# Optimization experiments

Measured on AMD Instinct MI355X. Metric: run time of the kernel, lower is better.

Reference implementation:

```python
import jax, jax.numpy as jnp
import numpy as np

N_EMBD = 1024
N_HEAD = 16


def setup_inputs() -> dict:
    key = jax.random.key(0)
    k1, k2, k3 = jax.random.split(key, 3)
    B, T, C = 4, 2048, N_EMBD
    x = jax.random.normal(k1, (B, T, C), dtype=jnp.float32)
    # params (bias=False)
    w_attn = jax.random.normal(k2, (C, 3 * C), dtype=jnp.float32) * (C ** -0.5)
    w_proj = jax.random.normal(k3, (C, C), dtype=jnp.float32) * (C ** -0.5)
    return {"x": x, "w_attn": w_attn, "w_proj": w_proj}


def reference(x, w_attn, w_proj):
    B, T, C = x.shape
    H = N_HEAD
    hs = C // H
    qkv = x @ w_attn  # [B,T,3C]
    q, k, v = jnp.split(qkv, 3, axis=-1)
    # [B,H,T,hs]
    q = q.reshape(B, T, H, hs).transpose(0, 2, 1, 3)
    k = k.reshape(B, T, H, hs).transpose(0, 2, 1, 3)
    v = v.reshape(B, T, H, hs).transpose(0, 2, 1, 3)
    wei = jnp.einsum('bhqd,bhkd->bhqk', q, k) * (hs ** -0.5)
    causal = jnp.tril(jnp.ones((T, T), dtype=bool))
    wei = jnp.where(causal[None, None], wei, -jnp.inf)
    wei = jax.nn.softmax(wei, axis=-1)
    # dropout p=0.0 -> identity
    y = jnp.einsum('bhqk,bhkd->bhqd', wei, v)
    y = y.transpose(0, 2, 1, 3).reshape(B, T, C)
    return y @ w_proj
```

## Files before the change

### kernel.cpp

```cpp
#include <hip/hip_runtime.h>
#include <math.h>
#include <stdint.h>

#define B_BATCH 4
#define T_SEQ   2048
#define C_EMB   1024
#define NH      16
#define HS      64

typedef _Float16 half_t;
typedef __attribute__((ext_vector_type(8))) _Float16 half8;
typedef __attribute__((ext_vector_type(4))) _Float16 half4;
typedef __attribute__((ext_vector_type(2))) __fp16 pk16x2;
typedef __attribute__((ext_vector_type(4))) float f32x4;

static __device__ __forceinline__ f32x4 mfma_k16(half4 a, half4 b, f32x4 c) {
#if __has_builtin(__builtin_amdgcn_mfma_f32_16x16x16f16)
    return __builtin_amdgcn_mfma_f32_16x16x16f16(a, b, c, 0, 0, 0);
#else
    half8 a8 = {a.x, a.y, a.z, a.w, (_Float16)0, (_Float16)0, (_Float16)0, (_Float16)0};
    half8 b8 = {b.x, b.y, b.z, b.w, (_Float16)0, (_Float16)0, (_Float16)0, (_Float16)0};
    return __builtin_amdgcn_mfma_f32_16x16x32_f16(a8, b8, c, 0, 0, 0);
#endif
}

static __device__ __forceinline__ void stage16(const void* g, void* lds_base) {
#if __has_builtin(__builtin_amdgcn_global_load_lds)
    __builtin_amdgcn_global_load_lds(
        (const __attribute__((address_space(1))) void*)g,
        (__attribute__((address_space(3))) void*)lds_base, 16, 0, 0);
#else
    const int lane = threadIdx.x & 63;
    ((uint4*)lds_base)[lane] = *(const uint4*)g;
#endif
}

__global__ __launch_bounds__(256) void prep_kernel(const float* __restrict__ x,
                                                   half_t* __restrict__ xh,
                                                   const float* __restrict__ wa,
                                                   half_t* __restrict__ waT,
                                                   const float* __restrict__ wp,
                                                   half_t* __restrict__ wpT) {
    const int blk = blockIdx.x;
    const int tid = threadIdx.x;

    if (blk < 4096) {
        const int i = blk * 256 + tid;
        const float4 a = *(const float4*)(x + (size_t)i * 8);
        const float4 b = *(const float4*)(x + (size_t)i * 8 + 4);
        const pk16x2 h0 = __builtin_amdgcn_cvt_pkrtz(a.x, a.y);
        const pk16x2 h1 = __builtin_amdgcn_cvt_pkrtz(a.z, a.w);
        const pk16x2 h2 = __builtin_amdgcn_cvt_pkrtz(b.x, b.y);
        const pk16x2 h3 = __builtin_amdgcn_cvt_pkrtz(b.z, b.w);
        half8 o = {(_Float16)h0.x, (_Float16)h0.y, (_Float16)h1.x, (_Float16)h1.y,
                   (_Float16)h2.x, (_Float16)h2.y, (_Float16)h3.x, (_Float16)h3.y};
        *(half8*)(xh + (size_t)i * 8) = o;
        return;
    }

    const float* W;
    half_t* WT;
    int K, N, bb;
    if (blk < 4096 + 768) {
        bb = blk - 4096; W = wa; WT = waT; K = 1024; N = 3072;
    } else {
        bb = blk - 4864; W = wp; WT = wpT; K = 1024; N = 1024;
    }
    const int ntiles = N / 64;
    const int n0 = (bb % ntiles) * 64;
    const int k0 = (bb / ntiles) * 64;

    __shared__ float t[64][65];
    const int r = tid >> 4, c4 = (tid & 15) * 4;
#pragma unroll
    for (int p = 0; p < 4; ++p) {
        const float4 g = *(const float4*)(W + (size_t)(k0 + p * 16 + r) * N + n0 + c4);
        t[p * 16 + r][c4 + 0] = g.x;
        t[p * 16 + r][c4 + 1] = g.y;
        t[p * 16 + r][c4 + 2] = g.z;
        t[p * 16 + r][c4 + 3] = g.w;
    }
    __syncthreads();
#pragma unroll
    for (int p = 0; p < 4; ++p) {
        const int n = p * 16 + r;
        half4 s = {(_Float16)t[c4 + 0][n], (_Float16)t[c4 + 1][n],
                   (_Float16)t[c4 + 2][n], (_Float16)t[c4 + 3][n]};
        *(half4*)(WT + (size_t)(n0 + n) * K + k0 + c4) = s;
    }
}

#define BK2 64

__global__ __launch_bounds__(512, 2) void gemm256(const half_t* __restrict__ A,
                                                  const half_t* __restrict__ Bt,
                                                  half_t* __restrict__ Cout,
                                                  int M, int N, int K) {
    __shared__ __align__(16) half_t SM[65536];

    const int tid  = threadIdx.x;
    const int lane = tid & 63;
    const int wid  = tid >> 6;
    const int l16  = lane & 15;
    const int quad = lane >> 4;

    const int nwg = gridDim.x;
    const int cpx = nwg >> 3;
    const int bid = (blockIdx.x & 7) * cpx + (blockIdx.x >> 3);
    const int nbx = N >> 8;
    const int bx = bid % nbx;
    const int by = bid / nbx;
    const size_t m0 = (size_t)by << 8;
    const size_t n0 = (size_t)bx << 8;

    const int warpM = (wid >> 2) * 128;
    const int wn    = (wid & 3) * 64;
    const int NTk   = K >> 6;

    const int srow = tid >> 3;
    const int scsw = (tid & 7) ^ (srow & 7);
    const half_t* gAs = A  + (m0 + srow) * (size_t)K + scsw * 8;
    const half_t* gBs = Bt + (n0 + srow) * (size_t)K + scsw * 8;

    f32x4 acc[8][4];
#pragma unroll
    for (int i = 0; i < 8; ++i)
#pragma unroll
        for (int j = 0; j < 4; ++j) acc[i][j] = (f32x4){0.f, 0.f, 0.f, 0.f};

    auto ldA = [&](const half_t* Ab, int mt, int kk) -> half8 {
        const int r = warpM + mt * 16 + l16;
        const int c = (kk * 4 + quad) ^ (l16 & 7);
        return *(const half8*)(Ab + r * 64 + c * 8);
    };
    auto ldB = [&](const half_t* Bb, int nt, int kk) -> half8 {
        const int r = wn + nt * 16 + l16;
        const int c = (kk * 4 + quad) ^ (l16 & 7);
        return *(const half8*)(Bb + r * 64 + c * 8);
    };

#pragma unroll
    for (int s = 0; s < 4; ++s)
        stage16(gAs + (size_t)(s * 64) * K, SM + s * 4096 + wid * 512);
#pragma unroll
    for (int s = 0; s < 4; ++s)
        stage16(gBs + (size_t)(s * 64) * K, SM + 16384 + s * 4096 + wid * 512);
    if (NTk > 1) {
#pragma unroll
        for (int s = 0; s < 4; ++s)
            stage16(gBs + (size_t)(s * 64) * K + BK2, SM + 49152 + s * 4096 + wid * 512);
        asm volatile("s_waitcnt vmcnt(4)" ::: "memory");
    } else {
        asm volatile("s_waitcnt vmcnt(0)" ::: "memory");
    }
    __builtin_amdgcn_s_barrier();
    __builtin_amdgcn_sched_barrier(0);

    auto tile_body = [&](int t, half_t* Ac, half_t* Bc, half_t* An) {
        const int kA = (t + 1) * BK2;
        const int kB = (t + 2) * BK2;
        const bool doA = (t + 1) < NTk;
        const bool doB = (t + 2) < NTk;

        half8 fb[4][2];

        if (doA) {
            stage16(gAs + (size_t)(0 * 64) * K + kA, An + 0 * 4096 + wid * 512);
            stage16(gAs + (size_t)(1 * 64) * K + kA, An + 1 * 4096 + wid * 512);
        }
#pragma unroll
        for (int nt = 0; nt < 4; ++nt) {
            fb[nt][0] = ldB(Bc, nt, 0);
            fb[nt][1] = ldB(Bc, nt, 1);
        }
        {
            half8 a00 = ldA(Ac, 0, 0), a01 = ldA(Ac, 0, 1);
            half8 a10 = ldA(Ac, 1, 0), a11 = ldA(Ac, 1, 1);
            __builtin_amdgcn_s_barrier();
            __builtin_amdgcn_s_setprio(1);
#pragma unroll
            for (int nt = 0; nt < 4; ++nt) {
                acc[0][nt] = __builtin_amdgcn_mfma_f32_16x16x32_f16(a00, fb[nt][0], acc[0][nt], 0, 0, 0);
                acc[0][nt] = __builtin_amdgcn_mfma_f32_16x16x32_f16(a01, fb[nt][1], acc[0][nt], 0, 0, 0);
                acc[1][nt] = __builtin_amdgcn_mfma_f32_16x16x32_f16(a10, fb[nt][0], acc[1][nt], 0, 0, 0);
                acc[1][nt] = __builtin_amdgcn_mfma_f32_16x16x32_f16(a11, fb[nt][1], acc[1][nt], 0, 0, 0);
            }
            __builtin_amdgcn_s_setprio(0);
        }
        if (doA) {
            stage16(gAs + (size_t)(2 * 64) * K + kA, An + 2 * 4096 + wid * 512);
            stage16(gAs + (size_t)(3 * 64) * K + kA, An + 3 * 4096 + wid * 512);
        }
        {
            half8 a00 = ldA(Ac, 2, 0), a01 = ldA(Ac, 2, 1);
            half8 a10 = ldA(Ac, 3, 0), a11 = ldA(Ac, 3, 1);
            __builtin_amdgcn_s_barrier();
            __builtin_amdgcn_s_setprio(1);
#pragma unroll
            for (int nt = 0; nt < 4; ++nt) {
                acc[2][nt] = __builtin_amdgcn_mfma_f32_16x16x32_f16(a00, fb[nt][0], acc[2][nt], 0, 0, 0);
                acc[2][nt] = __builtin_amdgcn_mfma_f32_16x16x32_f16(a01, fb[nt][1], acc[2][nt], 0, 0, 0);
                acc[3][nt] = __builtin_amdgcn_mfma_f32_16x16x32_f16(a10, fb[nt][0], acc[3][nt], 0, 0, 0);
                acc[3][nt] = __builtin_amdgcn_mfma_f32_16x16x32_f16(a11, fb[nt][1], acc[3][nt], 0, 0, 0);
            }
            __builtin_amdgcn_s_setprio(0);
        }
        if (doB) {
            stage16(gBs + (size_t)(0 * 64) * K + kB, Bc + 0 * 4096 + wid * 512);
            stage16(gBs + (size_t)(1 * 64) * K + kB, Bc + 1 * 4096 + wid * 512);
        }
        {
            half8 a00 = ldA(Ac, 4, 0), a01 = ldA(Ac, 4, 1);
            half8 a10 = ldA(Ac, 5, 0), a11 = ldA(Ac, 5, 1);
            __builtin_amdgcn_s_barrier();
            __builtin_amdgcn_s_setprio(1);
#pragma unroll
            for (int nt = 0; nt < 4; ++nt) {
                acc[4][nt] = __builtin_amdgcn_mfma_f32_16x16x32_f16(a00, fb[nt][0], acc[4][nt], 0, 0, 0);
                acc[4][nt] = __builtin_amdgcn_mfma_f32_16x16x32_f16(a01, fb[nt][1], acc[4][nt], 0, 0, 0);
                acc[5][nt] = __builtin_amdgcn_mfma_f32_16x16x32_f16(a10, fb[nt][0], acc[5][nt], 0, 0, 0);
                acc[5][nt] = __builtin_amdgcn_mfma_f32_16x16x32_f16(a11, fb[nt][1], acc[5][nt], 0, 0, 0);
            }
            __builtin_amdgcn_s_setprio(0);
        }
        if (doB) {
            stage16(gBs + (size_t)(2 * 64) * K + kB, Bc + 2 * 4096 + wid * 512);
            stage16(gBs + (size_t)(3 * 64) * K + kB, Bc + 3 * 4096 + wid * 512);
        }
        {
            half8 a00 = ldA(Ac, 6, 0), a01 = ldA(Ac, 6, 1);
            half8 a10 = ldA(Ac, 7, 0), a11 = ldA(Ac, 7, 1);
            __builtin_amdgcn_s_barrier();
            __builtin_amdgcn_s_setprio(1);
#pragma unroll
            for (int nt = 0; nt < 4; ++nt) {
                acc[6][nt] = __builtin_amdgcn_mfma_f32_16x16x32_f16(a00, fb[nt][0], acc[6][nt], 0, 0, 0);
                acc[6][nt] = __builtin_amdgcn_mfma_f32_16x16x32_f16(a01, fb[nt][1], acc[6][nt], 0, 0, 0);
                acc[7][nt] = __builtin_amdgcn_mfma_f32_16x16x32_f16(a10, fb[nt][0], acc[7][nt], 0, 0, 0);
                acc[7][nt] = __builtin_amdgcn_mfma_f32_16x16x32_f16(a11, fb[nt][1], acc[7][nt], 0, 0, 0);
            }
            __builtin_amdgcn_s_setprio(0);
        }
        if (doB) {
            asm volatile("s_waitcnt vmcnt(4)" ::: "memory");
        } else if (doA) {
            asm volatile("s_waitcnt vmcnt(0)" ::: "memory");
        }
        __builtin_amdgcn_s_barrier();
        __builtin_amdgcn_sched_barrier(0);
    };

    for (int tt = 0; tt < NTk; tt += 2) {
        tile_body(tt, SM, SM + 16384, SM + 32768);
        if (tt + 1 < NTk)
            tile_body(tt + 1, SM + 32768, SM + 49152, SM);
    }

    __syncthreads();
    float* cw = (float*)SM + wid * 1024;
    const int rrow = lane >> 2;
    const int cseg = (lane & 3) * 16;
#pragma unroll
    for (int mt = 0; mt < 8; ++mt) {
#pragma unroll
        for (int nt = 0; nt < 4; ++nt)
            *(f32x4*)&cw[(nt * 16 + l16) * 16 + quad * 4] = acc[mt][nt];
        half_t tmp[16];
#pragma unroll
        for (int jj = 0; jj < 16; ++jj)
            tmp[jj] = (half_t)cw[(cseg + jj) * 16 + rrow];
        half_t* dst = Cout + (m0 + warpM + mt * 16 + rrow) * (size_t)N + n0 + wn + cseg;
        *(half8*)(dst)     = *(const half8*)(tmp);
        *(half8*)(dst + 8) = *(const half8*)(tmp + 8);
    }
}

__global__ __launch_bounds__(256) void gemm_bt_a64(const half_t* __restrict__ A,
                                                   const half_t* __restrict__ Bt,
                                                   float* __restrict__ Cout,
                                                   int M, int N, int K) {
    __shared__ half_t As[64 * 32];
    __shared__ half_t Bs[128 * 32];

    const int tid  = threadIdx.x;
    const int lane = tid & 63;
    const int wid  = tid >> 6;
    const int l16  = lane & 15;
    const int quad = lane >> 4;

    const int m0 = blockIdx.y * 64;
    const int n0 = blockIdx.x * 128;
    const int wm = (wid & 1) * 32;
    const int wn = (wid >> 1) * 64;

    const half_t* gA  = A  + (size_t)(m0 + wid * 16      + (lane >> 2)) * K + (lane & 3) * 8;
    const half_t* gB0 = Bt + (size_t)(n0 + wid * 16      + (lane >> 2)) * K + (lane & 3) * 8;
    const half_t* gB1 = Bt + (size_t)(n0 + wid * 16 + 64 + (lane >> 2)) * K + (lane & 3) * 8;

    half_t* lA  = As + (size_t)wid * 512;
    half_t* lB0 = Bs + (size_t)wid * 512;
    half_t* lB1 = Bs + (size_t)(wid + 4) * 512;

    f32x4 acc[2][4];
#pragma unroll
    for (int i = 0; i < 2; ++i)
#pragma unroll
        for (int j = 0; j < 4; ++j) acc[i][j] = (f32x4){0.f, 0.f, 0.f, 0.f};

    for (int k0 = 0; k0 < K; k0 += 32) {
        __syncthreads();
        stage16(gA + k0, lA);
        stage16(gB0 + k0, lB0);
        stage16(gB1 + k0, lB1);
        __syncthreads();

        half8 fa[2], fb[4];
#pragma unroll
        for (int mt = 0; mt < 2; ++mt)
            fa[mt] = *(const half8*)(As + (wm + mt * 16 + l16) * 32 + quad * 8);
#pragma unroll
        for (int nt = 0; nt < 4; ++nt)
            fb[nt] = *(const half8*)(Bs + (wn + nt * 16 + l16) * 32 + quad * 8);
#pragma unroll
        for (int mt = 0; mt < 2; ++mt)
#pragma unroll
            for (int nt = 0; nt < 4; ++nt)
                acc[mt][nt] = __builtin_amdgcn_mfma_f32_16x16x32_f16(
                    fa[mt], fb[nt], acc[mt][nt], 0, 0, 0);
    }

#pragma unroll
    for (int mt = 0; mt < 2; ++mt)
#pragma unroll
        for (int nt = 0; nt < 4; ++nt)
#pragma unroll
            for (int r = 0; r < 4; ++r) {
                const size_t row = m0 + wm + mt * 16 + quad * 4 + r;
                const size_t col = n0 + wn + nt * 16 + l16;
                Cout[row * N + col] = acc[mt][nt][r];
            }
}

#define SCALE_EXP2 0.18033688f

__global__ __launch_bounds__(256, 4) void attn_mfma(const half_t* __restrict__ qkv,
                                                    half_t* __restrict__ y) {
    __shared__ __align__(16) half_t Kl[64 * 64];
    __shared__ __align__(16) half_t Vt[64 * 64];
    __shared__ float Lstat[64];

    const int tid  = threadIdx.x;
    const int wid  = tid >> 6;
    const int lane = tid & 63;
    const int l16  = lane & 15;
    const int quad = lane >> 4;

    const int L = blockIdx.x;
    const int g = L & 63;
    const int s = L >> 6;
    const int h = g & 15;
    const int b = g >> 4;

    const size_t rs = 3 * C_EMB;
    const half_t* qb = qkv + (size_t)b * T_SEQ * rs + h * HS;
    const half_t* kb = qb + C_EMB;
    const half_t* vb = qb + 2 * C_EMB;

    const int srow = tid >> 2;
    const int scol = (tid & 3) * 16;
    const int sc2  = (tid & 3) * 2;
    const int rp   = tid & 31;
    const int dblk = tid >> 5;

    const int qrel = wid * 16 + l16;

    auto kswz = [&](int row, int chunk) -> half_t* {
        return Kl + row * 64 + ((chunk ^ (row & 7)) << 3);
    };
    auto vswz = [&](int row, int chunk) -> half_t* {
        return Vt + row * 64 + ((chunk ^ (row & 7)) << 3);
    };

#pragma unroll 1
    for (int j = 0; j < 2; ++j) {
        const int qh = (j == 0) ? (31 - s) : s;
        const int q0 = qh * 64;

        __syncthreads();
        {
            const half_t* src = qb + (size_t)(q0 + srow) * rs + scol;
            const half8 q0r = *(const half8*)(src);
            const half8 q1r = *(const half8*)(src + 8);
            *(half8*)kswz(srow, sc2)     = q0r;
            *(half8*)kswz(srow, sc2 + 1) = q1r;
        }
        half8 kp0, kp1;
        uint4 vpa, vpc;
        {
            const half_t* ksrc = kb + (size_t)srow * rs + scol;
            kp0 = *(const half8*)(ksrc);
            kp1 = *(const half8*)(ksrc + 8);
            const half_t* vsrc = vb + (size_t)(2 * rp) * rs + dblk * 8;
            vpa = *(const uint4*)(vsrc);
            vpc = *(const uint4*)(vsrc + rs);
        }
        __syncthreads();

        half8 aQ[2];
        aQ[0] = *(const half8*)kswz(wid * 16 + l16, quad);
        aQ[1] = *(const half8*)kswz(wid * 16 + l16, 4 + quad);

        f32x4 O[4];
#pragma unroll
        for (int dt = 0; dt < 4; ++dt) O[dt] = (f32x4){0.f, 0.f, 0.f, 0.f};
        float lw = 0.f;

        for (int kt = 0; kt <= qh; ++kt) {
            const bool diag = (kt == qh);
            __syncthreads();

            *(half8*)kswz(srow, sc2)     = kp0;
            *(half8*)kswz(srow, sc2 + 1) = kp1;
            {
                const uint32_t a0[4] = {vpa.x, vpa.y, vpa.z, vpa.w};
                const uint32_t c0[4] = {vpc.x, vpc.y, vpc.z, vpc.w};
#pragma unroll
                for (int u = 0; u < 4; ++u) {
                    const int d0 = dblk * 8 + 2 * u;
                    const uint32_t w0 = (a0[u] & 0xffffu) | (c0[u] << 16);
                    const uint32_t w1 = (a0[u] >> 16) | (c0[u] & 0xffff0000u);
                    *(uint32_t*)((unsigned short*)vswz(d0,     rp >> 2) + (rp & 3) * 2) = w0;
                    *(uint32_t*)((unsigned short*)vswz(d0 + 1, rp >> 2) + (rp & 3) * 2) = w1;
                }
            }
            __syncthreads();

            if (kt < qh) {
                const int kn = (kt + 1) * 64;
                const half_t* ksrc = kb + (size_t)(kn + srow) * rs + scol;
                kp0 = *(const half8*)(ksrc);
                kp1 = *(const half8*)(ksrc + 8);
                const half_t* vsrc = vb + (size_t)(kn + 2 * rp) * rs + dblk * 8;
                vpa = *(const uint4*)(vsrc);
                vpc = *(const uint4*)(vsrc + rs);
            }

#pragma unroll
            for (int mt = 0; mt < 4; ++mt) {
                const half8 aK0 = *(const half8*)kswz(mt * 16 + l16, quad);
                const half8 aK1 = *(const half8*)kswz(mt * 16 + l16, 4 + quad);
                f32x4 sa = (f32x4){0.f, 0.f, 0.f, 0.f};
                sa = __builtin_amdgcn_mfma_f32_16x16x32_f16(aK0, aQ[0], sa, 0, 0, 0);
                sa = __builtin_amdgcn_mfma_f32_16x16x32_f16(aK1, aQ[1], sa, 0, 0, 0);

                const int kbase = mt * 16 + quad * 4;
                float p[4];
#pragma unroll
                for (int r = 0; r < 4; ++r)
                    p[r] = __builtin_amdgcn_exp2f(sa[r] * SCALE_EXP2);
                if (diag) {
#pragma unroll
                    for (int r = 0; r < 4; ++r)
                        if (kbase + r > qrel) p[r] = 0.f;
                }
                lw += (p[0] + p[1]) + (p[2] + p[3]);

                const half4 pa = {(_Float16)p[0], (_Float16)p[1],
                                  (_Float16)p[2], (_Float16)p[3]};
#pragma unroll
                for (int dt = 0; dt < 4; ++dt) {
                    const half_t* pv = vswz(dt * 16 + l16, 2 * mt + (quad >> 1)) +
                                       (quad & 1) * 4;
                    const half4 bV = *(const half4*)pv;
                    O[dt] = mfma_k16(pa, bV, O[dt]);
                }
            }
        }

        lw += __shfl_xor(lw, 16);
        lw += __shfl_xor(lw, 32);
        if (quad == 0) Lstat[wid * 16 + l16] = lw;
        __syncthreads();
#pragma unroll
        for (int r = 0; r < 4; ++r) {
            const int rowl = wid * 16 + quad * 4 + r;
            const float inv = 1.f / Lstat[rowl];
#pragma unroll
            for (int dt = 0; dt < 4; ++dt)
                *(vswz(rowl, 2 * dt + (l16 >> 3)) + (l16 & 7)) =
                    (half_t)(O[dt][r] * inv);
        }
        __syncthreads();
        {
            half_t* dst = y + ((size_t)b * T_SEQ + q0 + srow) * C_EMB + h * HS + scol;
            *(half8*)(dst)     = *(const half8*)vswz(srow, sc2);
            *(half8*)(dst + 8) = *(const half8*)vswz(srow, sc2 + 1);
        }
    }
}

extern "C" void kernel_launch(void* const* d_in, const int* in_sizes, int n_in,
                              void* d_out, int out_size, void* d_ws, size_t ws_size,
                              hipStream_t stream) {
    const float* x      = (const float*)d_in[0];
    const float* w_attn = (const float*)d_in[1];
    const float* w_proj = (const float*)d_in[2];
    float* out = (float*)d_out;

    half_t* xh   = (half_t*)d_ws;
    half_t* waT  = xh   + (size_t)8192 * 1024;
    half_t* wpT  = waT  + (size_t)3072 * 1024;
    half_t* qkvh = wpT  + (size_t)1024 * 1024;
    half_t* yh   = qkvh + (size_t)8192 * 3072;

    prep_kernel<<<5120, 256, 0, stream>>>(x, xh, w_attn, waT, w_proj, wpT);

    gemm256<<<dim3(384), 512, 0, stream>>>(xh, waT, qkvh, 8192, 3072, 1024);

    attn_mfma<<<dim3(1024), 256, 0, stream>>>(qkvh, yh);

    gemm_bt_a64<<<dim3(8, 128), 256, 0, stream>>>(yh, wpT, out, 8192, 1024, 1024);
}
```

Measured before the change: 261.5 us.

## Shrink QKV GEMM tile to 128x256 and reuse it for output projection

Turns the 256x256 pipelined GEMM into a templated 128x256 variant with a smaller shared-memory footprint. The QKV projection now launches twice as many workgroups, for better occupancy and wave balance across CUs. The naive output-projection kernel is replaced by the same pipelined kernel with a float-output epilogue. Priority hints (s_setprio) are also added around the MFMA clusters in the attention kernel. In exchange, the smaller tile gives less operand reuse per block, and the float epilogue writes outputs as scattered scalar stores.

```diff
diff --git a/kernel.cpp b/kernel.cpp
--- a/kernel.cpp
+++ b/kernel.cpp
@@ -92,11 +92,12 @@
 
 #define BK2 64
 
-__global__ __launch_bounds__(512, 2) void gemm256(const half_t* __restrict__ A,
+template <typename OutT>
+__global__ __launch_bounds__(512, 2) void gemm128(const half_t* __restrict__ A,
                                                   const half_t* __restrict__ Bt,
-                                                  half_t* __restrict__ Cout,
+                                                  OutT* __restrict__ Cout,
                                                   int M, int N, int K) {
-    __shared__ __align__(16) half_t SM[65536];
+    __shared__ __align__(16) half_t SM[49152];
 
     const int tid  = threadIdx.x;
     const int lane = tid & 63;
@@ -110,10 +111,10 @@
     const int nbx = N >> 8;
     const int bx = bid % nbx;
     const int by = bid / nbx;
-    const size_t m0 = (size_t)by << 8;
+    const size_t m0 = (size_t)by << 7;
     const size_t n0 = (size_t)bx << 8;
 
-    const int warpM = (wid >> 2) * 128;
+    const int warpM = (wid >> 2) * 64;
     const int wn    = (wid & 3) * 64;
     const int NTk   = K >> 6;
 
@@ -122,9 +123,14 @@
     const half_t* gAs = A  + (m0 + srow) * (size_t)K + scsw * 8;
     const half_t* gBs = Bt + (n0 + srow) * (size_t)K + scsw * 8;
 
-    f32x4 acc[8][4];
-#pragma unroll
-    for (int i = 0; i < 8; ++i)
+    half_t* const A0 = SM;
+    half_t* const B0 = SM + 8192;
+    half_t* const A1 = SM + 24576;
+    half_t* const B1 = SM + 32768;
+
+    f32x4 acc[4][4];
+#pragma unroll
+    for (int i = 0; i < 4; ++i)
 #pragma unroll
         for (int j = 0; j < 4; ++j) acc[i][j] = (f32x4){0.f, 0.f, 0.f, 0.f};
 
@@ -140,15 +146,15 @@
     };
 
 #pragma unroll
+    for (int s = 0; s < 2; ++s)
+        stage16(gAs + (size_t)(s * 64) * K, A0 + s * 4096 + wid * 512);
+#pragma unroll
     for (int s = 0; s < 4; ++s)
-        stage16(gAs + (size_t)(s * 64) * K, SM + s * 4096 + wid * 512);
-#pragma unroll
-    for (int s = 0; s < 4; ++s)
-        stage16(gBs + (size_t)(s * 64) * K, SM + 16384 + s * 4096 + wid * 512);
+        stage16(gBs + (size_t)(s * 64) * K, B0 + s * 4096 + wid * 512);
     if (NTk > 1) {
 #pragma unroll
         for (int s = 0; s < 4; ++s)
-            stage16(gBs + (size_t)(s * 64) * K + BK2, SM + 49152 + s * 4096 + wid * 512);
+            stage16(gBs + (size_t)(s * 64) * K + BK2, B1 + s * 4096 + wid * 512);
         asm volatile("s_waitcnt vmcnt(4)" ::: "memory");
     } else {
         asm volatile("s_waitcnt vmcnt(0)" ::: "memory");
@@ -187,9 +193,10 @@
             }
             __builtin_amdgcn_s_setprio(0);
         }
-        if (doA) {
-            stage16(gAs + (size_t)(2 * 64) * K + kA, An + 2 * 4096 + wid * 512);
-            stage16(gAs + (size_t)(3 * 64) * K + kA, An + 3 * 4096 + wid * 512);
+        if (doB) {
+#pragma unroll
+            for (int s = 0; s < 4; ++s)
+                stage16(gBs + (size_t)(s * 64) * K + kB, Bc + s * 4096 + wid * 512);
         }
         {
             half8 a00 = ldA(Ac, 2, 0), a01 = ldA(Ac, 2, 1);
@@ -206,42 +213,6 @@
             __builtin_amdgcn_s_setprio(0);
         }
         if (doB) {
-            stage16(gBs + (size_t)(0 * 64) * K + kB, Bc + 0 * 4096 + wid * 512);
-            stage16(gBs + (size_t)(1 * 64) * K + kB, Bc + 1 * 4096 + wid * 512);
-        }
-        {
-            half8 a00 = ldA(Ac, 4, 0), a01 = ldA(Ac, 4, 1);
-            half8 a10 = ldA(Ac, 5, 0), a11 = ldA(Ac, 5, 1);
-            __builtin_amdgcn_s_barrier();
-            __builtin_amdgcn_s_setprio(1);
-#pragma unroll
-            for (int nt = 0; nt < 4; ++nt) {
-                acc[4][nt] = __builtin_amdgcn_mfma_f32_16x16x32_f16(a00, fb[nt][0], acc[4][nt], 0, 0, 0);
-                acc[4][nt] = __builtin_amdgcn_mfma_f32_16x16x32_f16(a01, fb[nt][1], acc[4][nt], 0, 0, 0);
-                acc[5][nt] = __builtin_amdgcn_mfma_f32_16x16x32_f16(a10, fb[nt][0], acc[5][nt], 0, 0, 0);
-                acc[5][nt] = __builtin_amdgcn_mfma_f32_16x16x32_f16(a11, fb[nt][1], acc[5][nt], 0, 0, 0);
-            }
-            __builtin_amdgcn_s_setprio(0);
-        }
-        if (doB) {
-            stage16(gBs + (size_t)(2 * 64) * K + kB, Bc + 2 * 4096 + wid * 512);
-            stage16(gBs + (size_t)(3 * 64) * K + kB, Bc + 3 * 4096 + wid * 512);
-        }
-        {
-            half8 a00 = ldA(Ac, 6, 0), a01 = ldA(Ac, 6, 1);
-            half8 a10 = ldA(Ac, 7, 0), a11 = ldA(Ac, 7, 1);
-            __builtin_amdgcn_s_barrier();
-            __builtin_amdgcn_s_setprio(1);
-#pragma unroll
-            for (int nt = 0; nt < 4; ++nt) {
-                acc[6][nt] = __builtin_amdgcn_mfma_f32_16x16x32_f16(a00, fb[nt][0], acc[6][nt], 0, 0, 0);
-                acc[6][nt] = __builtin_amdgcn_mfma_f32_16x16x32_f16(a01, fb[nt][1], acc[6][nt], 0, 0, 0);
-                acc[7][nt] = __builtin_amdgcn_mfma_f32_16x16x32_f16(a10, fb[nt][0], acc[7][nt], 0, 0, 0);
-                acc[7][nt] = __builtin_amdgcn_mfma_f32_16x16x32_f16(a11, fb[nt][1], acc[7][nt], 0, 0, 0);
-            }
-            __builtin_amdgcn_s_setprio(0);
-        }
-        if (doB) {
             asm volatile("s_waitcnt vmcnt(4)" ::: "memory");
         } else if (doA) {
             asm volatile("s_waitcnt vmcnt(0)" ::: "memory");
@@ -251,94 +222,41 @@
     };
 
     for (int tt = 0; tt < NTk; tt += 2) {
-        tile_body(tt, SM, SM + 16384, SM + 32768);
+        tile_body(tt, A0, B0, A1);
         if (tt + 1 < NTk)
-            tile_body(tt + 1, SM + 32768, SM + 49152, SM);
+            tile_body(tt + 1, A1, B1, A0);
     }
 
     __syncthreads();
-    float* cw = (float*)SM + wid * 1024;
-    const int rrow = lane >> 2;
-    const int cseg = (lane & 3) * 16;
-#pragma unroll
-    for (int mt = 0; mt < 8; ++mt) {
-#pragma unroll
-        for (int nt = 0; nt < 4; ++nt)
-            *(f32x4*)&cw[(nt * 16 + l16) * 16 + quad * 4] = acc[mt][nt];
-        half_t tmp[16];
-#pragma unroll
-        for (int jj = 0; jj < 16; ++jj)
-            tmp[jj] = (half_t)cw[(cseg + jj) * 16 + rrow];
-        half_t* dst = Cout + (m0 + warpM + mt * 16 + rrow) * (size_t)N + n0 + wn + cseg;
-        *(half8*)(dst)     = *(const half8*)(tmp);
-        *(half8*)(dst + 8) = *(const half8*)(tmp + 8);
-    }
-}
-
-__global__ __launch_bounds__(256) void gemm_bt_a64(const half_t* __restrict__ A,
-                                                   const half_t* __restrict__ Bt,
-                                                   float* __restrict__ Cout,
-                                                   int M, int N, int K) {
-    __shared__ half_t As[64 * 32];
-    __shared__ half_t Bs[128 * 32];
-
-    const int tid  = threadIdx.x;
-    const int lane = tid & 63;
-    const int wid  = tid >> 6;
-    const int l16  = lane & 15;
-    const int quad = lane >> 4;
-
-    const int m0 = blockIdx.y * 64;
-    const int n0 = blockIdx.x * 128;
-    const int wm = (wid & 1) * 32;
-    const int wn = (wid >> 1) * 64;
-
-    const half_t* gA  = A  + (size_t)(m0 + wid * 16      + (lane >> 2)) * K + (lane & 3) * 8;
-    const half_t* gB0 = Bt + (size_t)(n0 + wid * 16      + (lane >> 2)) * K + (lane & 3) * 8;
-    const half_t* gB1 = Bt + (size_t)(n0 + wid * 16 + 64 + (lane >> 2)) * K + (lane & 3) * 8;
-
-    half_t* lA  = As + (size_t)wid * 512;
-    half_t* lB0 = Bs + (size_t)wid * 512;
-    half_t* lB1 = Bs + (size_t)(wid + 4) * 512;
-
-    f32x4 acc[2][4];
-#pragma unroll
-    for (int i = 0; i < 2; ++i)
-#pragma unroll
-        for (int j = 0; j < 4; ++j) acc[i][j] = (f32x4){0.f, 0.f, 0.f, 0.f};
-
-    for (int k0 = 0; k0 < K; k0 += 32) {
-        __syncthreads();
-        stage16(gA + k0, lA);
-        stage16(gB0 + k0, lB0);
-        stage16(gB1 + k0, lB1);
-        __syncthreads();
-
-        half8 fa[2], fb[4];
-#pragma unroll
-        for (int mt = 0; mt < 2; ++mt)
-            fa[mt] = *(const half8*)(As + (wm + mt * 16 + l16) * 32 + quad * 8);
-#pragma unroll
-        for (int nt = 0; nt < 4; ++nt)
-            fb[nt] = *(const half8*)(Bs + (wn + nt * 16 + l16) * 32 + quad * 8);
-#pragma unroll
-        for (int mt = 0; mt < 2; ++mt)
+    if constexpr (sizeof(OutT) == 2) {
+        float* cw = (float*)SM + wid * 1024;
+        const int rrow = lane >> 2;
+        const int cseg = (lane & 3) * 16;
+#pragma unroll
+        for (int mt = 0; mt < 4; ++mt) {
 #pragma unroll
             for (int nt = 0; nt < 4; ++nt)
-                acc[mt][nt] = __builtin_amdgcn_mfma_f32_16x16x32_f16(
-                    fa[mt], fb[nt], acc[mt][nt], 0, 0, 0);
-    }
-
-#pragma unroll
-    for (int mt = 0; mt < 2; ++mt)
-#pragma unroll
-        for (int nt = 0; nt < 4; ++nt)
-#pragma unroll
-            for (int r = 0; r < 4; ++r) {
-                const size_t row = m0 + wm + mt * 16 + quad * 4 + r;
-                const size_t col = n0 + wn + nt * 16 + l16;
-                Cout[row * N + col] = acc[mt][nt][r];
-            }
+                *(f32x4*)&cw[(nt * 16 + l16) * 16 + quad * 4] = acc[mt][nt];
+            half_t tmp[16];
+#pragma unroll
+            for (int jj = 0; jj < 16; ++jj)
+                tmp[jj] = (half_t)cw[(cseg + jj) * 16 + rrow];
+            OutT* dst = Cout + (m0 + warpM + mt * 16 + rrow) * (size_t)N + n0 + wn + cseg;
+            *(half8*)(dst)     = *(const half8*)(tmp);
+            *(half8*)(dst + 8) = *(const half8*)(tmp + 8);
+        }
+    } else {
+#pragma unroll
+        for (int mt = 0; mt < 4; ++mt)
+#pragma unroll
+            for (int nt = 0; nt < 4; ++nt)
+#pragma unroll
+                for (int r = 0; r < 4; ++r) {
+                    const size_t row = m0 + warpM + mt * 16 + quad * 4 + r;
+                    const size_t col = n0 + wn + nt * 16 + l16;
+                    Cout[row * (size_t)N + col] = acc[mt][nt][r];
+                }
+    }
 }
 
 #define SCALE_EXP2 0.18033688f
@@ -450,8 +368,10 @@
                 const half8 aK0 = *(const half8*)kswz(mt * 16 + l16, quad);
                 const half8 aK1 = *(const half8*)kswz(mt * 16 + l16, 4 + quad);
                 f32x4 sa = (f32x4){0.f, 0.f, 0.f, 0.f};
+                __builtin_amdgcn_s_setprio(1);
                 sa = __builtin_amdgcn_mfma_f32_16x16x32_f16(aK0, aQ[0], sa, 0, 0, 0);
                 sa = __builtin_amdgcn_mfma_f32_16x16x32_f16(aK1, aQ[1], sa, 0, 0, 0);
+                __builtin_amdgcn_s_setprio(0);
 
                 const int kbase = mt * 16 + quad * 4;
                 float p[4];
@@ -467,6 +387,7 @@
 
                 const half4 pa = {(_Float16)p[0], (_Float16)p[1],
                                   (_Float16)p[2], (_Float16)p[3]};
+                __builtin_amdgcn_s_setprio(1);
 #pragma unroll
                 for (int dt = 0; dt < 4; ++dt) {
                     const half_t* pv = vswz(dt * 16 + l16, 2 * mt + (quad >> 1)) +
@@ -474,6 +395,7 @@
                     const half4 bV = *(const half4*)pv;
                     O[dt] = mfma_k16(pa, bV, O[dt]);
                 }
+                __builtin_amdgcn_s_setprio(0);
             }
         }
 
@@ -515,9 +437,9 @@
 
     prep_kernel<<<5120, 256, 0, stream>>>(x, xh, w_attn, waT, w_proj, wpT);
 
-    gemm256<<<dim3(384), 512, 0, stream>>>(xh, waT, qkvh, 8192, 3072, 1024);
+    gemm128<half_t><<<dim3(768), 512, 0, stream>>>(xh, waT, qkvh, 8192, 3072, 1024);
 
     attn_mfma<<<dim3(1024), 256, 0, stream>>>(qkvh, yh);
 
-    gemm_bt_a64<<<dim3(8, 128), 256, 0, stream>>>(yh, wpT, out, 8192, 1024, 1024);
-}
+    gemm128<float><<<dim3(256), 512, 0, stream>>>(yh, wpT, out, 8192, 1024, 1024);
+}
```

Result: no change. 264.8 us (+1.2%).

## Replace output projection GEMM with double-buffered 128x256 swizzled-LDS kernel

Applied to the files above, without the earlier changes.

Replaces the simple 64x128 single-buffered projection GEMM with a 512-thread 128x256 tile kernel. It uses XOR-swizzled LDS, double-buffered K tiles with prefetch interleaved into the MFMA phases, setprio and explicit vmcnt waits, and an XCD-aware block remap. The aim is to raise operand reuse, hide global-load latency and avoid per-tile full syncs. In exchange the kernel uses more LDS and registers, and the grid drops to 256 blocks, which lowers occupancy and leaves fewer blocks to spread across CUs.

```diff
diff --git a/kernel.cpp b/kernel.cpp
--- a/kernel.cpp
+++ b/kernel.cpp
@@ -275,12 +275,11 @@
     }
 }
 
-__global__ __launch_bounds__(256) void gemm_bt_a64(const half_t* __restrict__ A,
+__global__ __launch_bounds__(512, 2) void gemm128f(const half_t* __restrict__ A,
                                                    const half_t* __restrict__ Bt,
                                                    float* __restrict__ Cout,
                                                    int M, int N, int K) {
-    __shared__ half_t As[64 * 32];
-    __shared__ half_t Bs[128 * 32];
+    __shared__ __align__(16) half_t SM[49152];
 
     const int tid  = threadIdx.x;
     const int lane = tid & 63;
@@ -288,56 +287,137 @@
     const int l16  = lane & 15;
     const int quad = lane >> 4;
 
-    const int m0 = blockIdx.y * 64;
-    const int n0 = blockIdx.x * 128;
-    const int wm = (wid & 1) * 32;
-    const int wn = (wid >> 1) * 64;
-
-    const half_t* gA  = A  + (size_t)(m0 + wid * 16      + (lane >> 2)) * K + (lane & 3) * 8;
-    const half_t* gB0 = Bt + (size_t)(n0 + wid * 16      + (lane >> 2)) * K + (lane & 3) * 8;
-    const half_t* gB1 = Bt + (size_t)(n0 + wid * 16 + 64 + (lane >> 2)) * K + (lane & 3) * 8;
-
-    half_t* lA  = As + (size_t)wid * 512;
-    half_t* lB0 = Bs + (size_t)wid * 512;
-    half_t* lB1 = Bs + (size_t)(wid + 4) * 512;
-
-    f32x4 acc[2][4];
-#pragma unroll
-    for (int i = 0; i < 2; ++i)
+    const int nwg = gridDim.x;
+    const int cpx = nwg >> 3;
+    const int bid = (blockIdx.x & 7) * cpx + (blockIdx.x >> 3);
+    const int nbx = N >> 8;
+    const int bx = bid % nbx;
+    const int by = bid / nbx;
+    const size_t m0 = (size_t)by << 7;
+    const size_t n0 = (size_t)bx << 8;
+
+    const int warpM = (wid >> 2) * 64;
+    const int wn    = (wid & 3) * 64;
+    const int NTk   = K >> 6;
+
+    const int srow = tid >> 3;
+    const int scsw = (tid & 7) ^ (srow & 7);
+    const half_t* gAs = A  + (m0 + srow) * (size_t)K + scsw * 8;
+    const half_t* gBs = Bt + (n0 + srow) * (size_t)K + scsw * 8;
+
+    half_t* const A0 = SM;
+    half_t* const B0 = SM + 8192;
+    half_t* const A1 = SM + 24576;
+    half_t* const B1 = SM + 32768;
+
+    f32x4 acc[4][4];
+#pragma unroll
+    for (int i = 0; i < 4; ++i)
 #pragma unroll
         for (int j = 0; j < 4; ++j) acc[i][j] = (f32x4){0.f, 0.f, 0.f, 0.f};
 
-    for (int k0 = 0; k0 < K; k0 += 32) {
-        __syncthreads();
-        stage16(gA + k0, lA);
-        stage16(gB0 + k0, lB0);
-        stage16(gB1 + k0, lB1);
-        __syncthreads();
-
-        half8 fa[2], fb[4];
-#pragma unroll
-        for (int mt = 0; mt < 2; ++mt)
-            fa[mt] = *(const half8*)(As + (wm + mt * 16 + l16) * 32 + quad * 8);
+    auto ldA = [&](const half_t* Ab, int mt, int kk) -> half8 {
+        const int r = warpM + mt * 16 + l16;
+        const int c = (kk * 4 + quad) ^ (l16 & 7);
+        return *(const half8*)(Ab + r * 64 + c * 8);
+    };
+    auto ldB = [&](const half_t* Bb, int nt, int kk) -> half8 {
+        const int r = wn + nt * 16 + l16;
+        const int c = (kk * 4 + quad) ^ (l16 & 7);
+        return *(const half8*)(Bb + r * 64 + c * 8);
+    };
+
+#pragma unroll
+    for (int s = 0; s < 2; ++s)
+        stage16(gAs + (size_t)(s * 64) * K, A0 + s * 4096 + wid * 512);
+#pragma unroll
+    for (int s = 0; s < 4; ++s)
+        stage16(gBs + (size_t)(s * 64) * K, B0 + s * 4096 + wid * 512);
+    if (NTk > 1) {
+#pragma unroll
+        for (int s = 0; s < 4; ++s)
+            stage16(gBs + (size_t)(s * 64) * K + BK2, B1 + s * 4096 + wid * 512);
+        asm volatile("s_waitcnt vmcnt(4)" ::: "memory");
+    } else {
+        asm volatile("s_waitcnt vmcnt(0)" ::: "memory");
+    }
+    __builtin_amdgcn_s_barrier();
+    __builtin_amdgcn_sched_barrier(0);
+
+    auto tile_body = [&](int t, half_t* Ac, half_t* Bc, half_t* An) {
+        const int kA = (t + 1) * BK2;
+        const int kB = (t + 2) * BK2;
+        const bool doA = (t + 1) < NTk;
+        const bool doB = (t + 2) < NTk;
+
+        half8 fb[4][2];
+
+        if (doA) {
+            stage16(gAs + (size_t)(0 * 64) * K + kA, An + 0 * 4096 + wid * 512);
+            stage16(gAs + (size_t)(1 * 64) * K + kA, An + 1 * 4096 + wid * 512);
+        }
+#pragma unroll
+        for (int nt = 0; nt < 4; ++nt) {
+            fb[nt][0] = ldB(Bc, nt, 0);
+            fb[nt][1] = ldB(Bc, nt, 1);
+        }
+        {
+            half8 a00 = ldA(Ac, 0, 0), a01 = ldA(Ac, 0, 1);
+            half8 a10 = ldA(Ac, 1, 0), a11 = ldA(Ac, 1, 1);
+            __builtin_amdgcn_s_barrier();
+            __builtin_amdgcn_s_setprio(1);
+#pragma unroll
+            for (int nt = 0; nt < 4; ++nt) {
+                acc[0][nt] = __builtin_amdgcn_mfma_f32_16x16x32_f16(a00, fb[nt][0], acc[0][nt], 0, 0, 0);
+                acc[0][nt] = __builtin_amdgcn_mfma_f32_16x16x32_f16(a01, fb[nt][1], acc[0][nt], 0, 0, 0);
+                acc[1][nt] = __builtin_amdgcn_mfma_f32_16x16x32_f16(a10, fb[nt][0], acc[1][nt], 0, 0, 0);
+                acc[1][nt] = __builtin_amdgcn_mfma_f32_16x16x32_f16(a11, fb[nt][1], acc[1][nt], 0, 0, 0);
+            }
+            __builtin_amdgcn_s_setprio(0);
+        }
+        if (doB) {
+#pragma unroll
+            for (int s = 0; s < 4; ++s)
+                stage16(gBs + (size_t)(s * 64) * K + kB, Bc + s * 4096 + wid * 512);
+        }
+        {
+            half8 a00 = ldA(Ac, 2, 0), a01 = ldA(Ac, 2, 1);
+            half8 a10 = ldA(Ac, 3, 0), a11 = ldA(Ac, 3, 1);
+            __builtin_amdgcn_s_barrier();
+            __builtin_amdgcn_s_setprio(1);
+#pragma unroll
+            for (int nt = 0; nt < 4; ++nt) {
+                acc[2][nt] = __builtin_amdgcn_mfma_f32_16x16x32_f16(a00, fb[nt][0], acc[2][nt], 0, 0, 0);
+                acc[2][nt] = __builtin_amdgcn_mfma_f32_16x16x32_f16(a01, fb[nt][1], acc[2][nt], 0, 0, 0);
+                acc[3][nt] = __builtin_amdgcn_mfma_f32_16x16x32_f16(a10, fb[nt][0], acc[3][nt], 0, 0, 0);
+                acc[3][nt] = __builtin_amdgcn_mfma_f32_16x16x32_f16(a11, fb[nt][1], acc[3][nt], 0, 0, 0);
+            }
+            __builtin_amdgcn_s_setprio(0);
+        }
+        if (doB) {
+            asm volatile("s_waitcnt vmcnt(4)" ::: "memory");
+        } else if (doA) {
+            asm volatile("s_waitcnt vmcnt(0)" ::: "memory");
+        }
+        __builtin_amdgcn_s_barrier();
+        __builtin_amdgcn_sched_barrier(0);
+    };
+
+    for (int tt = 0; tt < NTk; tt += 2) {
+        tile_body(tt, A0, B0, A1);
+        if (tt + 1 < NTk)
+            tile_body(tt + 1, A1, B1, A0);
+    }
+
+#pragma unroll
+    for (int mt = 0; mt < 4; ++mt)
 #pragma unroll
         for (int nt = 0; nt < 4; ++nt)
-            fb[nt] = *(const half8*)(Bs + (wn + nt * 16 + l16) * 32 + quad * 8);
-#pragma unroll
-        for (int mt = 0; mt < 2; ++mt)
-#pragma unroll
-            for (int nt = 0; nt < 4; ++nt)
-                acc[mt][nt] = __builtin_amdgcn_mfma_f32_16x16x32_f16(
-                    fa[mt], fb[nt], acc[mt][nt], 0, 0, 0);
-    }
-
-#pragma unroll
-    for (int mt = 0; mt < 2; ++mt)
-#pragma unroll
-        for (int nt = 0; nt < 4; ++nt)
 #pragma unroll
             for (int r = 0; r < 4; ++r) {
-                const size_t row = m0 + wm + mt * 16 + quad * 4 + r;
+                const size_t row = m0 + warpM + mt * 16 + quad * 4 + r;
                 const size_t col = n0 + wn + nt * 16 + l16;
-                Cout[row * N + col] = acc[mt][nt][r];
+                Cout[row * (size_t)N + col] = acc[mt][nt][r];
             }
 }
 
@@ -519,5 +599,5 @@
 
     attn_mfma<<<dim3(1024), 256, 0, stream>>>(qkvh, yh);
 
-    gemm_bt_a64<<<dim3(8, 128), 256, 0, stream>>>(yh, wpT, out, 8192, 1024, 1024);
+    gemm128f<<<dim3(256), 512, 0, stream>>>(yh, wpT, out, 8192, 1024, 1024);
 }
```

Measured after the change: 253.7 us. 1.03x faster.
